# Optimization experiments

Measured on AMD Instinct MI355X. Metric: run time of the kernel, lower is better.

Reference implementation:

```python
import jax, jax.numpy as jnp
import numpy as np

DIM = 512
NUM_HEADS = 8
B, NW, W = 8, 64, 64  # batch, num_windows, window_size


def setup_inputs() -> dict:
    key = jax.random.key(0)
    k1, k2, k3 = jax.random.split(key, 3)
    x = jax.random.normal(k1, (B, NW, W, DIM), dtype=jnp.float32)
    w_qkv = jax.random.normal(k2, (DIM, 3 * DIM), dtype=jnp.float32) * (DIM ** -0.5)
    w_proj = jax.random.normal(k3, (DIM, DIM), dtype=jnp.float32) * (DIM ** -0.5)
    b_proj = jnp.zeros((DIM,), dtype=jnp.float32)
    return {"x": x, "w_qkv": w_qkv, "w_proj": w_proj, "b_proj": b_proj}


def reference(x, w_qkv, w_proj, b_proj):
    batch, nw, w, dim = x.shape
    heads = NUM_HEADS
    dh = dim // heads
    scale = dh ** -0.5
    # qkv projection (no bias): [B, nW, W, 3*dim]
    qkv = jnp.einsum('bnwc,cd->bnwd', x, w_qkv)
    # -> [B, nW, W, 3, H, dh] -> [3, B, H, nW, W, dh]
    qkv = qkv.reshape(batch, nw, w, 3, heads, dh)
    qkv = jnp.transpose(qkv, (3, 0, 4, 1, 2, 5))
    q, k, v = qkv[0], qkv[1], qkv[2]
    # attention logits per window: [B, H, nW, W, W]
    attn = jnp.einsum('bhnqd,bhnkd->bhnqk', q, k) * scale
    attn = jax.nn.softmax(attn, axis=-1)
    # [B, H, nW, W, dh]
    out = jnp.einsum('bhnqk,bhnkd->bhnqd', attn, v)
    # faithful raw reshape (no transpose), matching the TF source
    out = out.reshape(batch, nw, w, dim)
    return jnp.einsum('bnwc,cd->bnwd', out, w_proj) + b_proj
```

## Files before the change

kernel.cpp:

```cpp
#include <hip/hip_runtime.h>
#include <hip/hip_bf16.h>

typedef __bf16 bf16_t;
typedef __bf16 bf16x8 __attribute__((ext_vector_type(8)));
typedef float f32x4 __attribute__((ext_vector_type(4)));

__global__ __launch_bounds__(256) void transpose_cast_kernel(
    const float* __restrict__ src, bf16_t* __restrict__ dst, int R, int C)
{
    __shared__ float tile[32][33];
    const int bx = blockIdx.x;
    const int by = blockIdx.y;
    const int t  = threadIdx.x;
    const int i0 = t >> 5;
    const int j  = t & 31;
#pragma unroll
    for (int p = 0; p < 4; ++p) {
        int i = i0 + p * 8;
        tile[i][j] = src[(long)(by * 32 + i) * C + bx * 32 + j];
    }
    __syncthreads();
#pragma unroll
    for (int p = 0; p < 4; ++p) {
        int i = i0 + p * 8;
        dst[(long)(bx * 32 + i) * R + by * 32 + j] = (bf16_t)tile[j][i];
    }
}

__global__ __launch_bounds__(256) void qkv_attn_kernel(
    const float*  __restrict__ x,
    const bf16_t* __restrict__ wT,
    bf16_t* __restrict__ ao)
{
    __shared__ bf16_t arena1[64 * 72];
    __shared__ bf16_t arena2[192 * 72];

    bf16_t* const lXc = arena1;
    bf16_t* const lP  = arena1;
    bf16_t* const lW  = arena2;
    bf16_t* const lQ  = arena2;
    bf16_t* const lK  = arena2 + 64 * 72;
    bf16_t* const lVT = arena2 + 128 * 72;

    const int id  = blockIdx.x;
    const int xcd = id & 7;
    const int s   = id >> 3;
    const int wid = xcd * 64 + (s >> 3);
    const int h   = s & 7;

    const int bb  = wid >> 6;
    const int nw  = wid & 63;
    const float* xw = x + (long)wid * 64 * 512;

    const int t    = threadIdx.x;
    const int wave = t >> 6;
    const int lane = t & 63;
    const int lr   = lane & 15;
    const int q    = lane >> 4;

    const float scale = 0.125f;

    f32x4 acc[12];
#pragma unroll
    for (int j = 0; j < 12; ++j) acc[j] = (f32x4)0.0f;

    for (int kc = 0; kc < 8; ++kc) {
        const int k0 = kc * 64;
#pragma unroll
        for (int p = 0; p < 2; ++p) {
            const int v = t + p * 256;
            const int r = v >> 3, c = (v & 7) * 8;
            const float* rp = xw + (long)r * 512 + k0 + c;
            f32x4 f0 = *(const f32x4*)rp;
            f32x4 f1 = *(const f32x4*)(rp + 4);
            bf16x8 o;
            o[0] = (bf16_t)f0[0]; o[1] = (bf16_t)f0[1];
            o[2] = (bf16_t)f0[2]; o[3] = (bf16_t)f0[3];
            o[4] = (bf16_t)f1[0]; o[5] = (bf16_t)f1[1];
            o[6] = (bf16_t)f1[2]; o[7] = (bf16_t)f1[3];
            *(bf16x8*)&lXc[r * 72 + c] = o;
        }
#pragma unroll
        for (int p = 0; p < 6; ++p) {
            const int v = t + p * 256;
            const int nr = v >> 3, c = (v & 7) * 8;
            const int g = nr >> 6, i = nr & 63;
            *(bf16x8*)&lW[nr * 72 + c] =
                *(const bf16x8*)(wT + (long)(g * 512 + h * 64 + i) * 512 + k0 + c);
        }
        __syncthreads();
#pragma unroll
        for (int ks = 0; ks < 64; ks += 32) {
            bf16x8 af = *(const bf16x8*)&lXc[(wave * 16 + lr) * 72 + ks + q * 8];
#pragma unroll
            for (int j = 0; j < 12; ++j) {
                bf16x8 bf = *(const bf16x8*)&lW[(j * 16 + lr) * 72 + ks + q * 8];
                acc[j] = __builtin_amdgcn_mfma_f32_16x16x32_bf16(af, bf, acc[j], 0, 0, 0);
            }
        }
        __syncthreads();
    }

#pragma unroll
    for (int j = 0; j < 4; ++j)
#pragma unroll
        for (int reg = 0; reg < 4; ++reg) {
            const int row = wave * 16 + q * 4 + reg;
            lQ[row * 72 + j * 16 + lr] = (bf16_t)acc[j][reg];
        }
#pragma unroll
    for (int j = 4; j < 8; ++j)
#pragma unroll
        for (int reg = 0; reg < 4; ++reg) {
            const int row = wave * 16 + q * 4 + reg;
            lK[row * 72 + (j - 4) * 16 + lr] = (bf16_t)acc[j][reg];
        }
#pragma unroll
    for (int j = 8; j < 12; ++j)
#pragma unroll
        for (int reg = 0; reg < 4; ++reg) {
            const int row = wave * 16 + q * 4 + reg;
            lVT[((j - 8) * 16 + lr) * 72 + row] = (bf16_t)acc[j][reg];
        }
    __syncthreads();

    f32x4 sAcc[4];
#pragma unroll
    for (int j = 0; j < 4; ++j) sAcc[j] = (f32x4)0.0f;
#pragma unroll
    for (int ks = 0; ks < 64; ks += 32) {
        bf16x8 aq = *(const bf16x8*)&lQ[(wave * 16 + lr) * 72 + ks + q * 8];
#pragma unroll
        for (int j = 0; j < 4; ++j) {
            bf16x8 bk = *(const bf16x8*)&lK[(j * 16 + lr) * 72 + ks + q * 8];
            sAcc[j] = __builtin_amdgcn_mfma_f32_16x16x32_bf16(aq, bk, sAcc[j], 0, 0, 0);
        }
    }

#pragma unroll
    for (int reg = 0; reg < 4; ++reg) {
        float m = fmaxf(fmaxf(sAcc[0][reg], sAcc[1][reg]),
                        fmaxf(sAcc[2][reg], sAcc[3][reg]));
#pragma unroll
        for (int d = 1; d < 16; d <<= 1) m = fmaxf(m, __shfl_xor(m, d));
        float p[4];
        float sum = 0.0f;
#pragma unroll
        for (int j = 0; j < 4; ++j) {
            p[j] = __expf((sAcc[j][reg] - m) * scale);
            sum += p[j];
        }
#pragma unroll
        for (int d = 1; d < 16; d <<= 1) sum += __shfl_xor(sum, d);
        const float inv = 1.0f / sum;
        const int row = wave * 16 + q * 4 + reg;
#pragma unroll
        for (int j = 0; j < 4; ++j)
            lP[row * 72 + j * 16 + lr] = (bf16_t)(p[j] * inv);
    }

    f32x4 o[4];
#pragma unroll
    for (int d4 = 0; d4 < 4; ++d4) o[d4] = (f32x4)0.0f;
#pragma unroll
    for (int ks = 0; ks < 64; ks += 32) {
        bf16x8 ap = *(const bf16x8*)&lP[(wave * 16 + lr) * 72 + ks + q * 8];
#pragma unroll
        for (int d4 = 0; d4 < 4; ++d4) {
            bf16x8 bv = *(const bf16x8*)&lVT[(d4 * 16 + lr) * 72 + ks + q * 8];
            o[d4] = __builtin_amdgcn_mfma_f32_16x16x32_bf16(ap, bv, o[d4], 0, 0, 0);
        }
    }

    bf16_t* aop = ao + ((long)bb * 4096 + (long)h * 512 + nw * 8) * 512;
#pragma unroll
    for (int d4 = 0; d4 < 4; ++d4)
#pragma unroll
        for (int reg = 0; reg < 4; ++reg) {
            const int wr = wave * 16 + q * 4 + reg;
            aop[(long)(wr >> 3) * 512 + (wr & 7) * 64 + d4 * 16 + lr] =
                (bf16_t)o[d4][reg];
        }
}

#define LDP 72

__global__ __launch_bounds__(256) void gemm2_kernel(
    const bf16_t* __restrict__ A,
    const bf16_t* __restrict__ Bt,
    const float*  __restrict__ bias,
    float* __restrict__ C,
    int M, int N, int K)
{
    __shared__ bf16_t lA[128 * LDP];
    __shared__ bf16_t lB[128 * LDP];

    const int tid  = threadIdx.x;
    const int wave = tid >> 6;
    const int lane = tid & 63;
    const int wm   = wave >> 1;
    const int wn   = wave & 1;
    const int lr   = lane & 15;
    const int q    = lane >> 4;

    const int id  = blockIdx.x;
    const int xcd = id & 7;
    const int s   = id >> 3;
    const int bm  = xcd * 32 + (s >> 2);
    const int bn  = s & 3;

    const long arow0 = (long)bm * 128;
    const long brow0 = (long)bn * 128;

    f32x4 acc[4][4];
#pragma unroll
    for (int i = 0; i < 4; ++i)
#pragma unroll
        for (int j = 0; j < 4; ++j) acc[i][j] = (f32x4)0.0f;

    const int srow = tid >> 3;
    const int scol = (tid & 7) * 8;

    const int nk = K / 64;
    for (int kt = 0; kt < nk; ++kt) {
        const bf16_t* Ag = A + arow0 * K + kt * 64;
        const bf16_t* Bg = Bt + brow0 * K + kt * 64;
        bf16x8 av[4], bv[4];
#pragma unroll
        for (int p = 0; p < 4; ++p) {
            const int r = srow + p * 32;
            av[p] = *(const bf16x8*)(Ag + (long)r * K + scol);
            bv[p] = *(const bf16x8*)(Bg + (long)r * K + scol);
        }
#pragma unroll
        for (int p = 0; p < 4; ++p) {
            const int r = srow + p * 32;
            *(bf16x8*)&lA[r * LDP + scol] = av[p];
            *(bf16x8*)&lB[r * LDP + scol] = bv[p];
        }
        __syncthreads();
#pragma unroll
        for (int ks = 0; ks < 64; ks += 32) {
            bf16x8 af[4], bf[4];
#pragma unroll
            for (int i = 0; i < 4; ++i)
                af[i] = *(const bf16x8*)&lA[(wm * 64 + i * 16 + lr) * LDP + ks + q * 8];
#pragma unroll
            for (int j = 0; j < 4; ++j)
                bf[j] = *(const bf16x8*)&lB[(wn * 64 + j * 16 + lr) * LDP + ks + q * 8];
#pragma unroll
            for (int i = 0; i < 4; ++i)
#pragma unroll
                for (int j = 0; j < 4; ++j)
                    acc[i][j] = __builtin_amdgcn_mfma_f32_16x16x32_bf16(
                        af[i], bf[j], acc[i][j], 0, 0, 0);
        }
        __syncthreads();
    }

#pragma unroll
    for (int i = 0; i < 4; ++i) {
        const long r = arow0 + wm * 64 + i * 16 + q * 4;
#pragma unroll
        for (int j = 0; j < 4; ++j) {
            const long c = brow0 + wn * 64 + j * 16 + lr;
            const float bv2 = bias[c];
#pragma unroll
            for (int reg = 0; reg < 4; ++reg) {
                C[(r + reg) * N + c] = acc[i][j][reg] + bv2;
            }
        }
    }
}

extern "C" void kernel_launch(void* const* d_in, const int* in_sizes, int n_in,
                              void* d_out, int out_size, void* d_ws, size_t ws_size,
                              hipStream_t stream)
{
    (void)in_sizes; (void)n_in; (void)out_size; (void)ws_size;
    const float* x     = (const float*)d_in[0];
    const float* wqkv  = (const float*)d_in[1];
    const float* wproj = (const float*)d_in[2];
    const float* bproj = (const float*)d_in[3];
    float* out = (float*)d_out;

    bf16_t* wT = (bf16_t*)d_ws;
    bf16_t* pT = wT + (size_t)1536 * 512;
    bf16_t* ao = pT + (size_t)512 * 512;

    transpose_cast_kernel<<<dim3(48, 16), 256, 0, stream>>>(wqkv, wT, 512, 1536);
    transpose_cast_kernel<<<dim3(16, 16), 256, 0, stream>>>(wproj, pT, 512, 512);

    qkv_attn_kernel<<<4096, 256, 0, stream>>>(x, wT, ao);

    gemm2_kernel<<<1024, 256, 0, stream>>>(
        ao, pT, bproj, out, 32768, 512, 512);
}
```

Measured before the change: 229.9 us.

## Process two windows per block with 32x32 MFMA, swizzled LDS, direct-to-LDS weight loads

Each qkv_attn block now handles two windows for one head, so every weight tile loaded into LDS is reused across 128 token rows instead of 64, and the grid is halved. The QKV projection switches to 32x32x16 MFMA tiles on a 2x2 wave grid. Padded LDS rows are replaced by an XOR swizzle, and weight tiles are copied with global_load_lds, bypassing registers. The cost is 64 KB of LDS per block and heavier register use, which may limit occupancy despite the launch-bounds hint of two blocks.

Measured after the change: 234.3 us. No clear change (+1.9%).

```diff
diff --git a/kernel.cpp b/kernel.cpp
--- a/kernel.cpp
+++ b/kernel.cpp
@@ -4,6 +4,15 @@
 typedef __bf16 bf16_t;
 typedef __bf16 bf16x8 __attribute__((ext_vector_type(8)));
 typedef float f32x4 __attribute__((ext_vector_type(4)));
+typedef float f32x16 __attribute__((ext_vector_type(16)));
+
+#define GLOAD_LDS16(gp, lp) __builtin_amdgcn_global_load_lds( \
+    (const __attribute__((address_space(1))) void*)(gp),      \
+    (__attribute__((address_space(3))) void*)(lp), 16, 0, 0)
+
+__device__ __forceinline__ int swz64(int row, int col) {
+    return row * 64 + (col ^ ((row & 7) << 3));
+}
 
 __global__ __launch_bounds__(256) void transpose_cast_kernel(
     const float* __restrict__ src, bf16_t* __restrict__ dst, int R, int C)
@@ -27,50 +36,51 @@
     }
 }
 
-__global__ __launch_bounds__(256) void qkv_attn_kernel(
+__global__ __launch_bounds__(256, 2) void qkv_attn_kernel(
     const float*  __restrict__ x,
     const bf16_t* __restrict__ wT,
     bf16_t* __restrict__ ao)
 {
-    __shared__ bf16_t arena1[64 * 72];
-    __shared__ bf16_t arena2[192 * 72];
-
-    bf16_t* const lXc = arena1;
-    bf16_t* const lP  = arena1;
-    bf16_t* const lW  = arena2;
-    bf16_t* const lQ  = arena2;
-    bf16_t* const lK  = arena2 + 64 * 72;
-    bf16_t* const lVT = arena2 + 128 * 72;
-
-    const int id  = blockIdx.x;
-    const int xcd = id & 7;
-    const int s   = id >> 3;
-    const int wid = xcd * 64 + (s >> 3);
-    const int h   = s & 7;
-
-    const int bb  = wid >> 6;
-    const int nw  = wid & 63;
-    const float* xw = x + (long)wid * 64 * 512;
+    __shared__ bf16_t arena[32768];
+    bf16_t* const lX = arena;
+    bf16_t* const lW = arena + 8192;
+
+    const int id   = blockIdx.x;
+    const int xcd  = id & 7;
+    const int s    = id >> 3;
+    const int pr   = xcd * 32 + (s >> 3);
+    const int h    = s & 7;
+    const int wid0 = pr * 2;
+
+    const float* xw = x + (long)wid0 * 64 * 512;
 
     const int t    = threadIdx.x;
-    const int wave = t >> 6;
+    const int wv   = t >> 6;
     const int lane = t & 63;
-    const int lr   = lane & 15;
-    const int q    = lane >> 4;
-
-    const float scale = 0.125f;
-
-    f32x4 acc[12];
-#pragma unroll
-    for (int j = 0; j < 12; ++j) acc[j] = (f32x4)0.0f;
+    const int wm   = wv >> 1;
+    const int wn   = wv & 1;
+    const int l31  = lane & 31;
+    const int l5   = lane >> 5;
+
+    bf16_t* const lQw = arena +     0 + wm * 12288;
+    bf16_t* const lKw = arena +  4096 + wm * 12288;
+    bf16_t* const lVw = arena +  8192 + wm * 12288;
+    bf16_t* const lPw = arena + 24576 + wm * 4096;
+
+    f32x16 acc[2][3];
+#pragma unroll
+    for (int mi = 0; mi < 2; ++mi)
+#pragma unroll
+        for (int ni = 0; ni < 3; ++ni) acc[mi][ni] = (f32x16)0.0f;
 
     for (int kc = 0; kc < 8; ++kc) {
         const int k0 = kc * 64;
 #pragma unroll
-        for (int p = 0; p < 2; ++p) {
-            const int v = t + p * 256;
-            const int r = v >> 3, c = (v & 7) * 8;
-            const float* rp = xw + (long)r * 512 + k0 + c;
+        for (int p = 0; p < 4; ++p) {
+            const int v  = t + p * 256;
+            const int r  = v >> 3;
+            const int sl = v & 7;
+            const float* rp = xw + (long)r * 512 + k0 + sl * 8;
             f32x4 f0 = *(const f32x4*)rp;
             f32x4 f1 = *(const f32x4*)(rp + 4);
             bf16x8 o;
@@ -78,109 +88,131 @@
             o[2] = (bf16_t)f0[2]; o[3] = (bf16_t)f0[3];
             o[4] = (bf16_t)f1[0]; o[5] = (bf16_t)f1[1];
             o[6] = (bf16_t)f1[2]; o[7] = (bf16_t)f1[3];
-            *(bf16x8*)&lXc[r * 72 + c] = o;
-        }
-#pragma unroll
-        for (int p = 0; p < 6; ++p) {
-            const int v = t + p * 256;
-            const int nr = v >> 3, c = (v & 7) * 8;
-            const int g = nr >> 6, i = nr & 63;
-            *(bf16x8*)&lW[nr * 72 + c] =
-                *(const bf16x8*)(wT + (long)(g * 512 + h * 64 + i) * 512 + k0 + c);
+            *(bf16x8*)&lX[r * 64 + ((sl ^ (r & 7)) * 8)] = o;
+        }
+        {
+            const int lsub = lane >> 3;
+            const int sl   = lane & 7;
+#pragma unroll
+            for (int j = 0; j < 6; ++j) {
+                const int rb   = wv * 6 + j;
+                const int nr   = rb * 8 + lsub;
+                const int ch   = sl ^ (nr & 7);
+                const int grow = ((nr >> 6) << 9) + h * 64 + (nr & 63);
+                GLOAD_LDS16(wT + (long)grow * 512 + k0 + ch * 8, &lW[rb * 512]);
+            }
         }
         __syncthreads();
 #pragma unroll
-        for (int ks = 0; ks < 64; ks += 32) {
-            bf16x8 af = *(const bf16x8*)&lXc[(wave * 16 + lr) * 72 + ks + q * 8];
-#pragma unroll
-            for (int j = 0; j < 12; ++j) {
-                bf16x8 bf = *(const bf16x8*)&lW[(j * 16 + lr) * 72 + ks + q * 8];
-                acc[j] = __builtin_amdgcn_mfma_f32_16x16x32_bf16(af, bf, acc[j], 0, 0, 0);
+        for (int ks = 0; ks < 64; ks += 16) {
+            bf16x8 a0 = *(const bf16x8*)&lX[swz64(wm * 64 +  0 + l31, ks + l5 * 8)];
+            bf16x8 a1 = *(const bf16x8*)&lX[swz64(wm * 64 + 32 + l31, ks + l5 * 8)];
+#pragma unroll
+            for (int ni = 0; ni < 3; ++ni) {
+                bf16x8 b = *(const bf16x8*)&lW[swz64(wn * 96 + ni * 32 + l31, ks + l5 * 8)];
+                acc[0][ni] = __builtin_amdgcn_mfma_f32_32x32x16_bf16(a0, b, acc[0][ni], 0, 0, 0);
+                acc[1][ni] = __builtin_amdgcn_mfma_f32_32x32x16_bf16(a1, b, acc[1][ni], 0, 0, 0);
             }
         }
         __syncthreads();
     }
 
 #pragma unroll
-    for (int j = 0; j < 4; ++j)
-#pragma unroll
-        for (int reg = 0; reg < 4; ++reg) {
-            const int row = wave * 16 + q * 4 + reg;
-            lQ[row * 72 + j * 16 + lr] = (bf16_t)acc[j][reg];
-        }
-#pragma unroll
-    for (int j = 4; j < 8; ++j)
-#pragma unroll
-        for (int reg = 0; reg < 4; ++reg) {
-            const int row = wave * 16 + q * 4 + reg;
-            lK[row * 72 + (j - 4) * 16 + lr] = (bf16_t)acc[j][reg];
-        }
-#pragma unroll
-    for (int j = 8; j < 12; ++j)
-#pragma unroll
-        for (int reg = 0; reg < 4; ++reg) {
-            const int row = wave * 16 + q * 4 + reg;
-            lVT[((j - 8) * 16 + lr) * 72 + row] = (bf16_t)acc[j][reg];
-        }
+    for (int mi = 0; mi < 2; ++mi) {
+#pragma unroll
+        for (int ni = 0; ni < 3; ++ni) {
+            const int n = wn * 96 + ni * 32 + l31;
+            const int g = n >> 6;
+            const int c = n & 63;
+#pragma unroll
+            for (int r = 0; r < 16; ++r) {
+                const int tk = mi * 32 + (r & 3) + ((r >> 2) << 3) + (l5 << 2);
+                const bf16_t val = (bf16_t)acc[mi][ni][r];
+                if (g == 0)      lQw[swz64(tk, c)] = val;
+                else if (g == 1) lKw[swz64(tk, c)] = val;
+                else             lVw[swz64(c, tk)] = val;
+            }
+        }
+    }
     __syncthreads();
 
-    f32x4 sAcc[4];
-#pragma unroll
-    for (int j = 0; j < 4; ++j) sAcc[j] = (f32x4)0.0f;
+    const int lr = lane & 15;
+    const int q  = lane >> 4;
+    const int qh = wn * 32;
+    const float scale = 0.125f;
+
+    f32x4 sA[2][4];
+#pragma unroll
+    for (int i = 0; i < 2; ++i)
+#pragma unroll
+        for (int j = 0; j < 4; ++j) sA[i][j] = (f32x4)0.0f;
 #pragma unroll
     for (int ks = 0; ks < 64; ks += 32) {
-        bf16x8 aq = *(const bf16x8*)&lQ[(wave * 16 + lr) * 72 + ks + q * 8];
+        bf16x8 aq0 = *(const bf16x8*)&lQw[swz64(qh +  0 + lr, ks + q * 8)];
+        bf16x8 aq1 = *(const bf16x8*)&lQw[swz64(qh + 16 + lr, ks + q * 8)];
 #pragma unroll
         for (int j = 0; j < 4; ++j) {
-            bf16x8 bk = *(const bf16x8*)&lK[(j * 16 + lr) * 72 + ks + q * 8];
-            sAcc[j] = __builtin_amdgcn_mfma_f32_16x16x32_bf16(aq, bk, sAcc[j], 0, 0, 0);
-        }
-    }
-
+            bf16x8 bk = *(const bf16x8*)&lKw[swz64(j * 16 + lr, ks + q * 8)];
+            sA[0][j] = __builtin_amdgcn_mfma_f32_16x16x32_bf16(aq0, bk, sA[0][j], 0, 0, 0);
+            sA[1][j] = __builtin_amdgcn_mfma_f32_16x16x32_bf16(aq1, bk, sA[1][j], 0, 0, 0);
+        }
+    }
+
+#pragma unroll
+    for (int i = 0; i < 2; ++i)
 #pragma unroll
     for (int reg = 0; reg < 4; ++reg) {
-        float m = fmaxf(fmaxf(sAcc[0][reg], sAcc[1][reg]),
-                        fmaxf(sAcc[2][reg], sAcc[3][reg]));
+        float m = fmaxf(fmaxf(sA[i][0][reg], sA[i][1][reg]),
+                        fmaxf(sA[i][2][reg], sA[i][3][reg]));
 #pragma unroll
         for (int d = 1; d < 16; d <<= 1) m = fmaxf(m, __shfl_xor(m, d));
         float p[4];
         float sum = 0.0f;
 #pragma unroll
         for (int j = 0; j < 4; ++j) {
-            p[j] = __expf((sAcc[j][reg] - m) * scale);
+            p[j] = __expf((sA[i][j][reg] - m) * scale);
             sum += p[j];
         }
 #pragma unroll
         for (int d = 1; d < 16; d <<= 1) sum += __shfl_xor(sum, d);
         const float inv = 1.0f / sum;
-        const int row = wave * 16 + q * 4 + reg;
+        const int row = qh + i * 16 + q * 4 + reg;
 #pragma unroll
         for (int j = 0; j < 4; ++j)
-            lP[row * 72 + j * 16 + lr] = (bf16_t)(p[j] * inv);
-    }
-
-    f32x4 o[4];
-#pragma unroll
-    for (int d4 = 0; d4 < 4; ++d4) o[d4] = (f32x4)0.0f;
+            lPw[swz64(row, j * 16 + lr)] = (bf16_t)(p[j] * inv);
+    }
+
+    f32x4 o[2][4];
+#pragma unroll
+    for (int i = 0; i < 2; ++i)
+#pragma unroll
+        for (int d4 = 0; d4 < 4; ++d4) o[i][d4] = (f32x4)0.0f;
 #pragma unroll
     for (int ks = 0; ks < 64; ks += 32) {
-        bf16x8 ap = *(const bf16x8*)&lP[(wave * 16 + lr) * 72 + ks + q * 8];
+        bf16x8 ap0 = *(const bf16x8*)&lPw[swz64(qh +  0 + lr, ks + q * 8)];
+        bf16x8 ap1 = *(const bf16x8*)&lPw[swz64(qh + 16 + lr, ks + q * 8)];
 #pragma unroll
         for (int d4 = 0; d4 < 4; ++d4) {
-            bf16x8 bv = *(const bf16x8*)&lVT[(d4 * 16 + lr) * 72 + ks + q * 8];
-            o[d4] = __builtin_amdgcn_mfma_f32_16x16x32_bf16(ap, bv, o[d4], 0, 0, 0);
-        }
-    }
-
+            bf16x8 bv = *(const bf16x8*)&lVw[swz64(d4 * 16 + lr, ks + q * 8)];
+            o[0][d4] = __builtin_amdgcn_mfma_f32_16x16x32_bf16(ap0, bv, o[0][d4], 0, 0, 0);
+            o[1][d4] = __builtin_amdgcn_mfma_f32_16x16x32_bf16(ap1, bv, o[1][d4], 0, 0, 0);
+        }
+    }
+
+    const int wid = wid0 + wm;
+    const int bb  = wid >> 6;
+    const int nw  = wid & 63;
     bf16_t* aop = ao + ((long)bb * 4096 + (long)h * 512 + nw * 8) * 512;
 #pragma unroll
+    for (int i = 0; i < 2; ++i)
+#pragma unroll
     for (int d4 = 0; d4 < 4; ++d4)
 #pragma unroll
-        for (int reg = 0; reg < 4; ++reg) {
-            const int wr = wave * 16 + q * 4 + reg;
-            aop[(long)(wr >> 3) * 512 + (wr & 7) * 64 + d4 * 16 + lr] =
-                (bf16_t)o[d4][reg];
-        }
+    for (int reg = 0; reg < 4; ++reg) {
+        const int wr = qh + i * 16 + q * 4 + reg;
+        aop[(long)(wr >> 3) * 512 + (wr & 7) * 64 + d4 * 16 + lr] =
+            (bf16_t)o[i][d4][reg];
+    }
 }
 
 #define LDP 72
@@ -291,7 +323,7 @@
     transpose_cast_kernel<<<dim3(48, 16), 256, 0, stream>>>(wqkv, wT, 512, 1536);
     transpose_cast_kernel<<<dim3(16, 16), 256, 0, stream>>>(wproj, pT, 512, 512);
 
-    qkv_attn_kernel<<<4096, 256, 0, stream>>>(x, wT, ao);
+    qkv_attn_kernel<<<2048, 256, 0, stream>>>(x, wT, ao);
 
     gemm2_kernel<<<1024, 256, 0, stream>>>(
         ao, pT, bproj, out, 32768, 512, 512);
```
